# Kernel optimization log

Hardware: AMD Instinct MI355X
Metric: run time of the kernel (lower is better)

The kernel has to match this reference:

```python
import jax, jax.numpy as jnp
import numpy as np

N = 50000
E = 800000
EPS = 1e-5


def graph_conv(x, src, dst, ew, W_rel, b_rel, W_root):
    # PyG GraphConv (aggr='add'): lin_rel(sum_j e_ij * x_j) + lin_root(x_i)
    msg = x[src] * ew[:, None]                      # [E, F_in]
    agg = jax.ops.segment_sum(msg, dst, num_segments=N)  # [N, F_in]
    return agg @ W_rel.T + b_rel + x @ W_root.T


def batchnorm_relu(h, gamma, beta):
    mu = jnp.mean(h, axis=0)
    var = jnp.mean(jnp.square(h - mu), axis=0)
    hn = (h - mu) * jax.lax.rsqrt(var + EPS)
    return jax.nn.relu(hn * gamma + beta)


def setup_inputs() -> dict:
    key = jax.random.key(0)
    ks = jax.random.split(key, 16)
    d_in, h, d_out = 128, 256, 64

    def lin(k, fo, fi):
        return jax.random.normal(k, (fo, fi), jnp.float32) * (1.0 / np.sqrt(fi))

    return {
        "x": jax.random.normal(ks[0], (N, d_in), jnp.float32),
        "edge_index": jax.random.randint(ks[1], (2, E), 0, N, jnp.int32),
        "edge_weight": jax.random.uniform(ks[2], (E,), jnp.float32),
        "Wr0": lin(ks[3], h, d_in), "br0": jnp.zeros((h,), jnp.float32), "Wt0": lin(ks[4], h, d_in),
        "g0": jnp.ones((h,), jnp.float32), "be0": jnp.zeros((h,), jnp.float32),
        "Wr1": lin(ks[5], h, h), "br1": jnp.zeros((h,), jnp.float32), "Wt1": lin(ks[6], h, h),
        "g1": jnp.ones((h,), jnp.float32), "be1": jnp.zeros((h,), jnp.float32),
        "Wr2": lin(ks[7], d_out, h), "br2": jnp.zeros((d_out,), jnp.float32), "Wt2": lin(ks[8], d_out, h),
    }


def reference(x, edge_index, edge_weight, Wr0, br0, Wt0, g0, be0,
              Wr1, br1, Wt1, g1, be1, Wr2, br2, Wt2):
    src, dst = edge_index[0], edge_index[1]
    h = graph_conv(x, src, dst, edge_weight, Wr0, br0, Wt0)
    h = batchnorm_relu(h, g0, be0)
    h = graph_conv(h, src, dst, edge_weight, Wr1, br1, Wt1)
    h = batchnorm_relu(h, g1, be1)
    return graph_conv(h, src, dst, edge_weight, Wr2, br2, Wt2)
```

## Files before the change

### kernel.cpp

```cpp
#include <hip/hip_runtime.h>
#include <cstddef>
#include <cstdint>

#define SCAN_B 512

using bf16x8 = __attribute__((ext_vector_type(8))) short;
using f32x4  = __attribute__((ext_vector_type(4))) float;

__device__ __forceinline__ unsigned short f2bf(float f) {
    unsigned int u = __builtin_bit_cast(unsigned int, f);
    return (unsigned short)((u + 0x7FFFu + ((u >> 16) & 1u)) >> 16);
}
__device__ __forceinline__ float bf2f(unsigned short b) {
    unsigned int u = ((unsigned int)b) << 16;
    return __builtin_bit_cast(float, u);
}
__device__ __forceinline__ float i2f(int i) { return __builtin_bit_cast(float, i); }
__device__ __forceinline__ float u2f(unsigned int u) { return __builtin_bit_cast(float, u); }
__device__ __forceinline__ void gload_lds16(const void* g, void* l) {
    __builtin_amdgcn_global_load_lds((const __attribute__((address_space(1))) void*)g,
                                     (__attribute__((address_space(3))) void*)l, 16, 0, 0);
}

__global__ void hist_conv_k(const int* __restrict__ dst, int* __restrict__ counts,
                            int* __restrict__ rank, int E, int histBlocks,
                            const float* __restrict__ x, const float* __restrict__ Wr0,
                            const float* __restrict__ Wt0, const float* __restrict__ Wr1,
                            const float* __restrict__ Wt1, const float* __restrict__ Wr2,
                            const float* __restrict__ Wt2, unsigned short* __restrict__ x_bf,
                            unsigned short* __restrict__ Wr0b, unsigned short* __restrict__ Wt0b,
                            unsigned short* __restrict__ Wr1b, unsigned short* __restrict__ Wt1b,
                            unsigned short* __restrict__ Wr2b, unsigned short* __restrict__ Wt2b,
                            int n4x) {
    if ((int)blockIdx.x < histBlocks) {
        int e = blockIdx.x * 256 + threadIdx.x;
        if (e < E) rank[e] = atomicAdd(&counts[dst[e]], 1);
        return;
    }
    int j = (blockIdx.x - histBlocks) * 256 + threadIdx.x;
    const float* s;
    unsigned short* d;
    if (j < n4x) { s = x; d = x_bf; }
    else {
        j -= n4x;
        if (j < 8192) { s = Wr0; d = Wr0b; }
        else { j -= 8192;
        if (j < 8192) { s = Wt0; d = Wt0b; }
        else { j -= 8192;
        if (j < 16384) { s = Wr1; d = Wr1b; }
        else { j -= 16384;
        if (j < 16384) { s = Wt1; d = Wt1b; }
        else { j -= 16384;
        if (j < 4096) { s = Wr2; d = Wr2b; }
        else { j -= 4096;
        if (j >= 4096) return;
        s = Wt2; d = Wt2b; } } } } }
    }
    float4 v = reinterpret_cast<const float4*>(s)[j];
    ushort4 o;
    o.x = f2bf(v.x); o.y = f2bf(v.y); o.z = f2bf(v.z); o.w = f2bf(v.w);
    reinterpret_cast<ushort4*>(d)[j] = o;
}

__global__ void scan1_k(const int* __restrict__ counts, int* __restrict__ partial,
                        int* __restrict__ blocksum, int Nn) {
    __shared__ int sh[SCAN_B];
    int i = blockIdx.x * SCAN_B + threadIdx.x;
    int v = (i < Nn) ? counts[i] : 0;
    sh[threadIdx.x] = v;
    __syncthreads();
    for (int off = 1; off < SCAN_B; off <<= 1) {
        int t = (threadIdx.x >= (unsigned)off) ? sh[threadIdx.x - off] : 0;
        __syncthreads();
        sh[threadIdx.x] += t;
        __syncthreads();
    }
    if (i < Nn) partial[i] = sh[threadIdx.x];
    if (threadIdx.x == SCAN_B - 1) blocksum[blockIdx.x] = sh[threadIdx.x];
}

__global__ void scan3b_k(const int* __restrict__ partial, const int* __restrict__ blocksum,
                         int* __restrict__ offsets, int Nn) {
    __shared__ int add_s;
    int bx = blockIdx.x;
    if (threadIdx.x < 64) {
        int s = 0;
        for (int j = threadIdx.x; j < bx; j += 64) s += blocksum[j];
        #pragma unroll
        for (int off = 32; off > 0; off >>= 1) s += __shfl_down(s, off, 64);
        if (threadIdx.x == 0) add_s = s;
    }
    __syncthreads();
    int i = bx * SCAN_B + threadIdx.x;
    if (i >= Nn) return;
    offsets[i + 1] = partial[i] + add_s;
    if (i == 0) offsets[0] = 0;
}

__global__ void fill2_k(const int* __restrict__ src, const int* __restrict__ dst,
                        const float* __restrict__ ew, const int* __restrict__ offsets,
                        const int* __restrict__ rank, int2* __restrict__ e_sw, int E) {
    int e = blockIdx.x * blockDim.x + threadIdx.x;
    if (e >= E) return;
    int pos = offsets[dst[e]] + rank[e];
    e_sw[pos] = make_int2(src[e], __builtin_bit_cast(int, ew[e]));
}

__global__ void gather128_k(const unsigned short* __restrict__ x, const int* __restrict__ offsets,
                            const int2* __restrict__ e_sw, unsigned short* __restrict__ agg, int Nn) {
    int wid = __builtin_amdgcn_readfirstlane((blockIdx.x * blockDim.x + threadIdx.x) >> 6);
    int lane = threadIdx.x & 63;
    if (wid >= Nn) return;
    int p = offsets[wid], end = offsets[wid + 1];
    const char* xb = (const char*)x;
    const unsigned loff = lane * 4u;
    float a0 = 0.f, a1 = 0.f;
    for (; p + 8 <= end; p += 8) {
        int2 ee[8];
        #pragma unroll
        for (int i = 0; i < 8; ++i) ee[i] = e_sw[p + i];
        unsigned vv[8];
        #pragma unroll
        for (int i = 0; i < 8; ++i)
            vv[i] = *reinterpret_cast<const unsigned*>(xb + ((unsigned)ee[i].x * 256u + loff));
        #pragma unroll
        for (int i = 0; i < 8; ++i) {
            float w = i2f(ee[i].y);
            a0 += w * u2f(vv[i] << 16); a1 += w * u2f(vv[i] & 0xFFFF0000u);
        }
    }
    for (; p < end; ++p) {
        int2 e0 = e_sw[p];
        unsigned v0 = *reinterpret_cast<const unsigned*>(xb + ((unsigned)e0.x * 256u + loff));
        float w = i2f(e0.y);
        a0 += w * u2f(v0 << 16); a1 += w * u2f(v0 & 0xFFFF0000u);
    }
    unsigned o = (unsigned)f2bf(a0) | ((unsigned)f2bf(a1) << 16);
    *reinterpret_cast<unsigned*>(agg + (size_t)wid * 128 + lane * 2) = o;
}

__global__ void gather_bn_k(const unsigned short* __restrict__ h_raw,
                            const float* __restrict__ sums, const float* __restrict__ sumsq,
                            const float* __restrict__ g, const float* __restrict__ be,
                            const int* __restrict__ offsets, const int2* __restrict__ e_sw,
                            unsigned short* __restrict__ agg, unsigned short* __restrict__ hN,
                            float invN, int Nn) {
    const int lane = threadIdx.x & 63;
    const int bx = blockIdx.x;
    if (bx % 7 == 6) {
        int bidx = bx / 7;
        int nbn = (int)gridDim.x / 7;
        int total4 = Nn * 64;
        int stride = nbn * 256;
        for (int t = bidx * 256 + threadIdx.x; t < total4; t += stride) {
            int f0 = (t & 63) * 4;
            float4 sm = *reinterpret_cast<const float4*>(sums + f0);
            float4 sq = *reinterpret_cast<const float4*>(sumsq + f0);
            float4 gg = *reinterpret_cast<const float4*>(g + f0);
            float4 bb = *reinterpret_cast<const float4*>(be + f0);
            float smv[4] = {sm.x, sm.y, sm.z, sm.w};
            float sqv[4] = {sq.x, sq.y, sq.z, sq.w};
            float ggv[4] = {gg.x, gg.y, gg.z, gg.w};
            float bbv[4] = {bb.x, bb.y, bb.z, bb.w};
            ushort4 v = reinterpret_cast<const ushort4*>(h_raw)[t];
            unsigned short vv[4] = {v.x, v.y, v.z, v.w};
            ushort4 o;
            unsigned short* op = &o.x;
            #pragma unroll
            for (int c = 0; c < 4; ++c) {
                float mu = smv[c] * invN;
                float var = sqv[c] * invN - mu * mu;
                float sc = ggv[c] * rsqrtf(var + 1e-5f);
                float sh = bbv[c] - mu * sc;
                op[c] = f2bf(fmaxf(bf2f(vv[c]) * sc + sh, 0.f));
            }
            reinterpret_cast<ushort4*>(hN)[t] = o;
        }
        return;
    }
    int gidx = bx - (bx + 1) / 7;
    int wid = __builtin_amdgcn_readfirstlane((gidx * 256 + (int)threadIdx.x) >> 6);
    if (wid >= Nn) return;
    int f0 = lane * 4;
    float4 sm = *reinterpret_cast<const float4*>(sums + f0);
    float4 sq = *reinterpret_cast<const float4*>(sumsq + f0);
    float4 gg = *reinterpret_cast<const float4*>(g + f0);
    float4 bb = *reinterpret_cast<const float4*>(be + f0);
    float sc0, sc1, sc2, sc3, sh0, sh1, sh2, sh3;
    {
        float mu, var;
        mu = sm.x * invN; var = sq.x * invN - mu * mu; sc0 = gg.x * rsqrtf(var + 1e-5f); sh0 = bb.x - mu * sc0;
        mu = sm.y * invN; var = sq.y * invN - mu * mu; sc1 = gg.y * rsqrtf(var + 1e-5f); sh1 = bb.y - mu * sc1;
        mu = sm.z * invN; var = sq.z * invN - mu * mu; sc2 = gg.z * rsqrtf(var + 1e-5f); sh2 = bb.z - mu * sc2;
        mu = sm.w * invN; var = sq.w * invN - mu * mu; sc3 = gg.w * rsqrtf(var + 1e-5f); sh3 = bb.w - mu * sc3;
    }
    int p = offsets[wid], end = offsets[wid + 1];
    const char* xb = (const char*)h_raw;
    const unsigned loff = lane * 8u;
    float a0 = 0.f, a1 = 0.f, a2 = 0.f, a3 = 0.f;
    for (; p + 8 <= end; p += 8) {
        int2 ee[8];
        #pragma unroll
        for (int i = 0; i < 8; ++i) ee[i] = e_sw[p + i];
        uint2 vv[8];
        #pragma unroll
        for (int i = 0; i < 8; ++i)
            vv[i] = *reinterpret_cast<const uint2*>(xb + ((unsigned)ee[i].x * 512u + loff));
        #pragma unroll
        for (int i = 0; i < 8; ++i) {
            float w = i2f(ee[i].y);
            a0 += w * fmaxf(u2f(vv[i].x << 16) * sc0 + sh0, 0.f);
            a1 += w * fmaxf(u2f(vv[i].x & 0xFFFF0000u) * sc1 + sh1, 0.f);
            a2 += w * fmaxf(u2f(vv[i].y << 16) * sc2 + sh2, 0.f);
            a3 += w * fmaxf(u2f(vv[i].y & 0xFFFF0000u) * sc3 + sh3, 0.f);
        }
    }
    for (; p < end; ++p) {
        int2 e0 = e_sw[p];
        uint2 v0 = *reinterpret_cast<const uint2*>(xb + ((unsigned)e0.x * 512u + loff));
        float w = i2f(e0.y);
        a0 += w * fmaxf(u2f(v0.x << 16) * sc0 + sh0, 0.f);
        a1 += w * fmaxf(u2f(v0.x & 0xFFFF0000u) * sc1 + sh1, 0.f);
        a2 += w * fmaxf(u2f(v0.y << 16) * sc2 + sh2, 0.f);
        a3 += w * fmaxf(u2f(v0.y & 0xFFFF0000u) * sc3 + sh3, 0.f);
    }
    uint2 o;
    o.x = (unsigned)f2bf(a0) | ((unsigned)f2bf(a1) << 16);
    o.y = (unsigned)f2bf(a2) | ((unsigned)f2bf(a3) << 16);
    *reinterpret_cast<uint2*>(agg + (size_t)wid * 256 + lane * 4) = o;
}

__global__ void gather_out_k(const unsigned short* __restrict__ t, const float* __restrict__ root,
                             const int* __restrict__ offsets, const int2* __restrict__ e_sw,
                             float* __restrict__ out, int Nn) {
    int gt = blockIdx.x * blockDim.x + threadIdx.x;
    int node = gt >> 4;
    int li = gt & 15;
    if (node >= Nn) return;
    int p = offsets[node], end = offsets[node + 1];
    const char* tb = (const char*)t;
    const unsigned loff = li * 8u;
    float a0 = 0.f, a1 = 0.f, a2 = 0.f, a3 = 0.f;
    for (; p + 8 <= end; p += 8) {
        int2 ee[8];
        #pragma unroll
        for (int i = 0; i < 8; ++i) ee[i] = e_sw[p + i];
        uint2 vv[8];
        #pragma unroll
        for (int i = 0; i < 8; ++i)
            vv[i] = *reinterpret_cast<const uint2*>(tb + ((unsigned)ee[i].x * 128u + loff));
        #pragma unroll
        for (int i = 0; i < 8; ++i) {
            float w = i2f(ee[i].y);
            a0 += w * u2f(vv[i].x << 16); a1 += w * u2f(vv[i].x & 0xFFFF0000u);
            a2 += w * u2f(vv[i].y << 16); a3 += w * u2f(vv[i].y & 0xFFFF0000u);
        }
    }
    for (; p < end; ++p) {
        int2 e0 = e_sw[p];
        uint2 v0 = *reinterpret_cast<const uint2*>(tb + ((unsigned)e0.x * 128u + loff));
        float w = i2f(e0.y);
        a0 += w * u2f(v0.x << 16); a1 += w * u2f(v0.x & 0xFFFF0000u);
        a2 += w * u2f(v0.y << 16); a3 += w * u2f(v0.y & 0xFFFF0000u);
    }
    float4 r = *reinterpret_cast<const float4*>(root + (size_t)node * 64 + li * 4);
    float4 o = make_float4(r.x + a0, r.y + a1, r.z + a2, r.w + a3);
    *reinterpret_cast<float4*>(out + (size_t)node * 64 + li * 4) = o;
}

template<int K, int O, int MODE>
__global__ __launch_bounds__(512, 4) void gemm_mfma_k(
        const unsigned short* __restrict__ A, const unsigned short* __restrict__ Wa,
        const unsigned short* __restrict__ X, const unsigned short* __restrict__ Wb,
        const float* __restrict__ bias, unsigned short* __restrict__ out_bf,
        float* __restrict__ out_f, float* __restrict__ sums, float* __restrict__ sumsq,
        int Nn) {
    constexpr int BM = 128, BN = 128;
    constexpr int MI = 4;
    constexpr int OJ = 2;
    constexpr int KSTEPS = K / 32;
    constexpr int NT = (MODE == 0 ? 2 : 1) * KSTEPS;
    __shared__ unsigned short As[2][BM * 32];
    __shared__ unsigned short Bs[2][BN * 32];
    const int tid = threadIdx.x;
    const int w = tid >> 6, l = tid & 63;
    const int wr = w >> 2, wc = w & 3;
    const int lrow = l & 15, kgrp = l >> 4;
    int bx = blockIdx.x;
    bx = (bx & 7) * (gridDim.x >> 3) + (bx >> 3);
    const int m0 = bx * BM;
    const int n0 = blockIdx.y * BN;
    const int srow = tid >> 2, sslot = tid & 3;
    const int gslot = sslot ^ ((srow >> 1) & 3);

    auto stage = [&](int buf, int t) {
        int ph = t / KSTEPS;
        int k0 = (t % KSTEPS) * 32;
        const unsigned short* Ap = (MODE == 0 && ph) ? X : A;
        const unsigned short* Wp = (MODE == 0 && ph) ? Wb : Wa;
        gload_lds16(Ap + (size_t)(m0 + srow) * K + k0 + (gslot << 3), &As[buf][w * 512]);
        gload_lds16(Wp + (size_t)(n0 + srow) * K + k0 + (gslot << 3), &Bs[buf][w * 512]);
    };

    f32x4 acc[MI][OJ];
    #pragma unroll
    for (int i = 0; i < MI; ++i)
        #pragma unroll
        for (int j = 0; j < OJ; ++j) {
            f32x4 z = {0.f, 0.f, 0.f, 0.f};
            acc[i][j] = z;
        }

    stage(0, 0);
    __syncthreads();
    #pragma unroll
    for (int t = 0; t < NT; ++t) {
        const int cur = t & 1;
        if (t + 1 < NT) stage(cur ^ 1, t + 1);
        bf16x8 a[MI], b[OJ];
        #pragma unroll
        for (int mi = 0; mi < MI; ++mi) {
            int row = wr * 64 + mi * 16 + lrow;
            int slot = kgrp ^ ((row >> 1) & 3);
            a[mi] = *reinterpret_cast<const bf16x8*>(&As[cur][row * 32 + slot * 8]);
        }
        #pragma unroll
        for (int oj = 0; oj < OJ; ++oj) {
            int row = wc * 32 + oj * 16 + lrow;
            int slot = kgrp ^ ((row >> 1) & 3);
            b[oj] = *reinterpret_cast<const bf16x8*>(&Bs[cur][row * 32 + slot * 8]);
        }
        #pragma unroll
        for (int mi = 0; mi < MI; ++mi)
            #pragma unroll
            for (int oj = 0; oj < OJ; ++oj)
                acc[mi][oj] = __builtin_amdgcn_mfma_f32_16x16x32_bf16(
                    a[mi], b[oj], acc[mi][oj], 0, 0, 0);
        __syncthreads();
    }

    #pragma unroll
    for (int oj = 0; oj < OJ; ++oj) {
        int col = n0 + wc * 32 + oj * 16 + lrow;
        float bcol = bias[col];
        float s = 0.f, q = 0.f;
        #pragma unroll
        for (int mi = 0; mi < MI; ++mi) {
            #pragma unroll
            for (int r = 0; r < 4; ++r) {
                int row = m0 + wr * 64 + mi * 16 + kgrp * 4 + r;
                float v = acc[mi][oj][r] + bcol;
                if (row < Nn) {
                    out_bf[(size_t)row * O + col] = f2bf(v);
                    s += v; q += v * v;
                }
            }
        }
        s += __shfl_xor(s, 16, 64); q += __shfl_xor(q, 16, 64);
        s += __shfl_xor(s, 32, 64); q += __shfl_xor(q, 32, 64);
        if (kgrp == 0) {
            atomicAdd(&sums[col], s);
            atomicAdd(&sumsq[col], q);
        }
    }
}

template<int K>
__global__ __launch_bounds__(512, 4) void gemm2_bn_k(
        const unsigned short* __restrict__ A, const unsigned short* __restrict__ Wa,
        const float* __restrict__ sums, const float* __restrict__ sumsq,
        const float* __restrict__ g, const float* __restrict__ be,
        const float* __restrict__ bias, unsigned short* __restrict__ t_bf,
        float* __restrict__ root, float invN, int Nn) {
    constexpr int BM = 128, BN = 128;
    constexpr int MI = 4, OJ = 2;
    constexpr int NT = K / 32;
    __shared__ unsigned short As[2][BM * 32];
    __shared__ unsigned short Bs[2][BN * 32];
    const int tid = threadIdx.x;
    const int w = tid >> 6, l = tid & 63;
    const int wr = w >> 2, wc = w & 3;
    const int lrow = l & 15, kgrp = l >> 4;
    int bx = blockIdx.x;
    bx = (bx & 7) * (gridDim.x >> 3) + (bx >> 3);
    const int m0 = bx * BM;
    const int srow = tid >> 2, sslot = tid & 3;
    const int gslot = sslot ^ ((srow >> 1) & 3);

    auto stageW = [&](int buf, int t) {
        gload_lds16(Wa + (size_t)srow * K + t * 32 + (gslot << 3), &Bs[buf][w * 512]);
    };
    auto loadA = [&](int t) -> bf16x8 {
        return *reinterpret_cast<const bf16x8*>(A + (size_t)(m0 + srow) * K + t * 32 + (gslot << 3));
    };
    auto writeA = [&](int buf, int t, bf16x8 raw) {
        int f0 = t * 32 + (gslot << 3);
        bf16x8 o;
        #pragma unroll
        for (int j = 0; j < 8; ++j) {
            int f = f0 + j;
            float mu = sums[f] * invN;
            float var = sumsq[f] * invN - mu * mu;
            float sc = g[f] * rsqrtf(var + 1e-5f);
            float sh = be[f] - mu * sc;
            float v = bf2f((unsigned short)raw[j]) * sc + sh;
            o[j] = (short)f2bf(fmaxf(v, 0.f));
        }
        *reinterpret_cast<bf16x8*>(&As[buf][tid * 8]) = o;
    };

    f32x4 acc[MI][OJ];
    #pragma unroll
    for (int i = 0; i < MI; ++i)
        #pragma unroll
        for (int j = 0; j < OJ; ++j) {
            f32x4 z = {0.f, 0.f, 0.f, 0.f};
            acc[i][j] = z;
        }

    {
        bf16x8 r0 = loadA(0);
        stageW(0, 0);
        writeA(0, 0, r0);
    }
    __syncthreads();
    #pragma unroll
    for (int t = 0; t < NT; ++t) {
        const int cur = t & 1;
        bf16x8 nxt;
        if (t + 1 < NT) { nxt = loadA(t + 1); stageW(cur ^ 1, t + 1); }
        bf16x8 a[MI], b[OJ];
        #pragma unroll
        for (int mi = 0; mi < MI; ++mi) {
            int row = wr * 64 + mi * 16 + lrow;
            int slot = kgrp ^ ((row >> 1) & 3);
            a[mi] = *reinterpret_cast<const bf16x8*>(&As[cur][row * 32 + slot * 8]);
        }
        #pragma unroll
        for (int oj = 0; oj < OJ; ++oj) {
            int row = wc * 32 + oj * 16 + lrow;
            int slot = kgrp ^ ((row >> 1) & 3);
            b[oj] = *reinterpret_cast<const bf16x8*>(&Bs[cur][row * 32 + slot * 8]);
        }
        #pragma unroll
        for (int mi = 0; mi < MI; ++mi)
            #pragma unroll
            for (int oj = 0; oj < OJ; ++oj)
                acc[mi][oj] = __builtin_amdgcn_mfma_f32_16x16x32_bf16(
                    a[mi], b[oj], acc[mi][oj], 0, 0, 0);
        if (t + 1 < NT) writeA(cur ^ 1, t + 1, nxt);
        __syncthreads();
    }

    #pragma unroll
    for (int oj = 0; oj < OJ; ++oj) {
        int col = wc * 32 + oj * 16 + lrow;
        #pragma unroll
        for (int mi = 0; mi < MI; ++mi) {
            #pragma unroll
            for (int r = 0; r < 4; ++r) {
                int row = m0 + wr * 64 + mi * 16 + kgrp * 4 + r;
                if (row < Nn) {
                    if (col < 64)
                        t_bf[(size_t)row * 64 + col] = f2bf(acc[mi][oj][r]);
                    else
                        root[(size_t)row * 64 + (col - 64)] = acc[mi][oj][r] + bias[col - 64];
                }
            }
        }
    }
}

extern "C" void kernel_launch(void* const* d_in, const int* in_sizes, int n_in,
                              void* d_out, int out_size, void* d_ws, size_t ws_size,
                              hipStream_t stream) {
    const float* x   = (const float*)d_in[0];
    const int*   ei  = (const int*)d_in[1];
    const float* ew  = (const float*)d_in[2];
    const float* Wr0 = (const float*)d_in[3];
    const float* br0 = (const float*)d_in[4];
    const float* Wt0 = (const float*)d_in[5];
    const float* g0  = (const float*)d_in[6];
    const float* be0 = (const float*)d_in[7];
    const float* Wr1 = (const float*)d_in[8];
    const float* br1 = (const float*)d_in[9];
    const float* Wt1 = (const float*)d_in[10];
    const float* g1  = (const float*)d_in[11];
    const float* be1 = (const float*)d_in[12];
    const float* Wr2 = (const float*)d_in[13];
    const float* br2 = (const float*)d_in[14];
    const float* Wt2 = (const float*)d_in[15];

    const int E  = in_sizes[2];
    const int Nn = in_sizes[0] / 128;
    const size_t NP = 50176;
    const int* src = ei;
    const int* dst = ei + E;

    unsigned short* x_bf   = (unsigned short*)d_ws;
    unsigned short* agg_bf = x_bf + NP * 128;
    unsigned short* h0N    = agg_bf + NP * 256;
    unsigned short* h1N    = h0N + NP * 256;
    unsigned short* h_bf   = h1N + NP * 256;
    unsigned short* t_bf   = h_bf + NP * 256;
    unsigned short* wbf    = t_bf + NP * 64;
    unsigned short* Wr0b = wbf;
    unsigned short* Wt0b = wbf + 32768;
    unsigned short* Wr1b = wbf + 65536;
    unsigned short* Wt1b = wbf + 131072;
    unsigned short* W2cat = wbf + 196608;
    float* root  = (float*)(wbf + 229376);
    int2*  e_sw  = (int2*)(root + NP * 64);
    float* stats = (float*)(e_sw + E);
    int*   counts  = (int*)(stats + 4096);
    int*   partial = counts + Nn;
    int*   blocksum = partial + Nn;
    int*   rank    = blocksum + 512;
    int*   offsets = rank + E;

    dim3 blk(256);
    const int nbScan = (Nn + SCAN_B - 1) / SCAN_B;
    const float invN = 1.0f / (float)Nn;
    const int n4x = Nn * 32;
    const int histBlocks = (E + 255) / 256;
    const int convBlocks = (n4x + 57344 + 255) / 256;

    hipMemsetAsync(stats, 0, (4096 + (size_t)Nn) * sizeof(float), stream);

    hist_conv_k<<<dim3(histBlocks + convBlocks), blk, 0, stream>>>(
        dst, counts, rank, E, histBlocks,
        x, Wr0, Wt0, Wr1, Wt1, Wr2, Wt2,
        x_bf, Wr0b, Wt0b, Wr1b, Wt1b, W2cat, W2cat + 16384, n4x);
    scan1_k<<<dim3(nbScan), dim3(SCAN_B), 0, stream>>>(counts, partial, blocksum, Nn);
    scan3b_k<<<dim3(nbScan), dim3(SCAN_B), 0, stream>>>(partial, blocksum, offsets, Nn);
    fill2_k<<<dim3(histBlocks), blk, 0, stream>>>(src, dst, ew, offsets, rank, e_sw, E);

    const int gatherBlocks = (Nn * 64 + 255) / 256;

    gather128_k<<<dim3(gatherBlocks), blk, 0, stream>>>(x_bf, offsets, e_sw, agg_bf, Nn);
    gemm_mfma_k<128, 256, 0><<<dim3(NP / 128, 2), dim3(512), 0, stream>>>(
        agg_bf, Wr0b, x_bf, Wt0b, br0, h_bf, nullptr, stats + 0, stats + 256, Nn);

    gather_bn_k<<<dim3(14584), blk, 0, stream>>>(
        h_bf, stats + 0, stats + 256, g0, be0, offsets, e_sw,
        agg_bf, h0N, invN, Nn);

    gemm_mfma_k<256, 256, 0><<<dim3(NP / 128, 2), dim3(512), 0, stream>>>(
        agg_bf, Wr1b, h0N, Wt1b, br1, h_bf, nullptr, stats + 1024, stats + 1280, Nn);

    gemm2_bn_k<256><<<dim3(NP / 128, 1), dim3(512), 0, stream>>>(
        h_bf, W2cat, stats + 1024, stats + 1280, g1, be1, br2, t_bf, root, invN, Nn);
    gather_out_k<<<dim3((Nn * 16 + 255) / 256), blk, 0, stream>>>(
        t_bf, root, offsets, e_sw, (float*)d_out, Nn);
}
```

Measured before the change: 293.5 us.

## Fuse layer-0 BN+ReLU into layer-1 GEMM root operand and precompute BN scales in LDS

Result: faster. 281.3 us (-4.1%).

```diff
diff --git a/kernel.cpp b/kernel.cpp
--- a/kernel.cpp
+++ b/kernel.cpp
@@ -143,43 +143,9 @@
                             const float* __restrict__ sums, const float* __restrict__ sumsq,
                             const float* __restrict__ g, const float* __restrict__ be,
                             const int* __restrict__ offsets, const int2* __restrict__ e_sw,
-                            unsigned short* __restrict__ agg, unsigned short* __restrict__ hN,
-                            float invN, int Nn) {
+                            unsigned short* __restrict__ agg, float invN, int Nn) {
     const int lane = threadIdx.x & 63;
-    const int bx = blockIdx.x;
-    if (bx % 7 == 6) {
-        int bidx = bx / 7;
-        int nbn = (int)gridDim.x / 7;
-        int total4 = Nn * 64;
-        int stride = nbn * 256;
-        for (int t = bidx * 256 + threadIdx.x; t < total4; t += stride) {
-            int f0 = (t & 63) * 4;
-            float4 sm = *reinterpret_cast<const float4*>(sums + f0);
-            float4 sq = *reinterpret_cast<const float4*>(sumsq + f0);
-            float4 gg = *reinterpret_cast<const float4*>(g + f0);
-            float4 bb = *reinterpret_cast<const float4*>(be + f0);
-            float smv[4] = {sm.x, sm.y, sm.z, sm.w};
-            float sqv[4] = {sq.x, sq.y, sq.z, sq.w};
-            float ggv[4] = {gg.x, gg.y, gg.z, gg.w};
-            float bbv[4] = {bb.x, bb.y, bb.z, bb.w};
-            ushort4 v = reinterpret_cast<const ushort4*>(h_raw)[t];
-            unsigned short vv[4] = {v.x, v.y, v.z, v.w};
-            ushort4 o;
-            unsigned short* op = &o.x;
-            #pragma unroll
-            for (int c = 0; c < 4; ++c) {
-                float mu = smv[c] * invN;
-                float var = sqv[c] * invN - mu * mu;
-                float sc = ggv[c] * rsqrtf(var + 1e-5f);
-                float sh = bbv[c] - mu * sc;
-                op[c] = f2bf(fmaxf(bf2f(vv[c]) * sc + sh, 0.f));
-            }
-            reinterpret_cast<ushort4*>(hN)[t] = o;
-        }
-        return;
-    }
-    int gidx = bx - (bx + 1) / 7;
-    int wid = __builtin_amdgcn_readfirstlane((gidx * 256 + (int)threadIdx.x) >> 6);
+    int wid = __builtin_amdgcn_readfirstlane((blockIdx.x * blockDim.x + threadIdx.x) >> 6);
     if (wid >= Nn) return;
     int f0 = lane * 4;
     float4 sm = *reinterpret_cast<const float4*>(sums + f0);
@@ -268,18 +234,16 @@
     *reinterpret_cast<float4*>(out + (size_t)node * 64 + li * 4) = o;
 }
 
-template<int K, int O, int MODE>
-__global__ __launch_bounds__(512, 4) void gemm_mfma_k(
+template<int K, int O>
+__global__ __launch_bounds__(512, 4) void gemm0_k(
         const unsigned short* __restrict__ A, const unsigned short* __restrict__ Wa,
         const unsigned short* __restrict__ X, const unsigned short* __restrict__ Wb,
         const float* __restrict__ bias, unsigned short* __restrict__ out_bf,
-        float* __restrict__ out_f, float* __restrict__ sums, float* __restrict__ sumsq,
-        int Nn) {
+        float* __restrict__ sums, float* __restrict__ sumsq, int Nn) {
     constexpr int BM = 128, BN = 128;
-    constexpr int MI = 4;
-    constexpr int OJ = 2;
+    constexpr int MI = 4, OJ = 2;
     constexpr int KSTEPS = K / 32;
-    constexpr int NT = (MODE == 0 ? 2 : 1) * KSTEPS;
+    constexpr int NT = 2 * KSTEPS;
     __shared__ unsigned short As[2][BM * 32];
     __shared__ unsigned short Bs[2][BN * 32];
     const int tid = threadIdx.x;
@@ -296,8 +260,8 @@
     auto stage = [&](int buf, int t) {
         int ph = t / KSTEPS;
         int k0 = (t % KSTEPS) * 32;
-        const unsigned short* Ap = (MODE == 0 && ph) ? X : A;
-        const unsigned short* Wp = (MODE == 0 && ph) ? Wb : Wa;
+        const unsigned short* Ap = ph ? X : A;
+        const unsigned short* Wp = ph ? Wb : Wa;
         gload_lds16(Ap + (size_t)(m0 + srow) * K + k0 + (gslot << 3), &As[buf][w * 512]);
         gload_lds16(Wp + (size_t)(n0 + srow) * K + k0 + (gslot << 3), &Bs[buf][w * 512]);
     };
@@ -361,6 +325,135 @@
         if (kgrp == 0) {
             atomicAdd(&sums[col], s);
             atomicAdd(&sumsq[col], q);
+        }
+    }
+}
+
+template<int K, int O>
+__global__ __launch_bounds__(512, 4) void gemm1_bn_k(
+        const unsigned short* __restrict__ A, const unsigned short* __restrict__ Wa,
+        const unsigned short* __restrict__ X, const unsigned short* __restrict__ Wb,
+        const float* __restrict__ sums0, const float* __restrict__ sumsq0,
+        const float* __restrict__ g0, const float* __restrict__ be0,
+        const float* __restrict__ bias, unsigned short* __restrict__ out_bf,
+        float* __restrict__ sums1, float* __restrict__ sumsq1, float invN, int Nn) {
+    constexpr int BM = 128, BN = 128;
+    constexpr int MI = 4, OJ = 2;
+    constexpr int KSTEPS = K / 32;
+    constexpr int NT = 2 * KSTEPS;
+    __shared__ unsigned short As[2][BM * 32];
+    __shared__ unsigned short Bs[2][BN * 32];
+    __shared__ float scs[256], shs[256];
+    const int tid = threadIdx.x;
+    const int w = tid >> 6, l = tid & 63;
+    const int wr = w >> 2, wc = w & 3;
+    const int lrow = l & 15, kgrp = l >> 4;
+    int bx = blockIdx.x;
+    bx = (bx & 7) * (gridDim.x >> 3) + (bx >> 3);
+    const int m0 = bx * BM;
+    const int n0 = blockIdx.y * BN;
+    const int srow = tid >> 2, sslot = tid & 3;
+    const int gslot = sslot ^ ((srow >> 1) & 3);
+
+    auto stageB = [&](int buf, int t) {
+        int k0 = (t % KSTEPS) * 32;
+        const unsigned short* Wp = (t < KSTEPS) ? Wa : Wb;
+        gload_lds16(Wp + (size_t)(n0 + srow) * K + k0 + (gslot << 3), &Bs[buf][w * 512]);
+    };
+    auto stageA = [&](int buf, int t) {
+        int k0 = t * 32;
+        gload_lds16(A + (size_t)(m0 + srow) * K + k0 + (gslot << 3), &As[buf][w * 512]);
+    };
+    auto loadX = [&](int t) -> bf16x8 {
+        int k0 = (t - KSTEPS) * 32;
+        return *reinterpret_cast<const bf16x8*>(X + (size_t)(m0 + srow) * K + k0 + (gslot << 3));
+    };
+    auto writeX = [&](int buf, int t, bf16x8 raw) {
+        int f0 = (t - KSTEPS) * 32 + (gslot << 3);
+        bf16x8 o;
+        #pragma unroll
+        for (int j = 0; j < 8; ++j) {
+            float v = bf2f((unsigned short)raw[j]) * scs[f0 + j] + shs[f0 + j];
+            o[j] = (short)f2bf(fmaxf(v, 0.f));
+        }
+        *reinterpret_cast<bf16x8*>(&As[buf][tid * 8]) = o;
+    };
+
+    if (tid < 256) {
+        float mu = sums0[tid] * invN;
+        float var = sumsq0[tid] * invN - mu * mu;
+        float sc = g0[tid] * rsqrtf(var + 1e-5f);
+        scs[tid] = sc;
+        shs[tid] = be0[tid] - mu * sc;
+    }
+
+    f32x4 acc[MI][OJ];
+    #pragma unroll
+    for (int i = 0; i < MI; ++i)
+        #pragma unroll
+        for (int j = 0; j < OJ; ++j) {
+            f32x4 z = {0.f, 0.f, 0.f, 0.f};
+            acc[i][j] = z;
+        }
+
+    stageB(0, 0);
+    stageA(0, 0);
+    __syncthreads();
+    #pragma unroll
+    for (int t = 0; t < NT; ++t) {
+        const int cur = t & 1;
+        bf16x8 nxt;
+        const bool nxtReg = (t + 1 < NT) && (t + 1 >= KSTEPS);
+        if (t + 1 < NT) {
+            stageB(cur ^ 1, t + 1);
+            if (t + 1 < KSTEPS) stageA(cur ^ 1, t + 1);
+            else nxt = loadX(t + 1);
+        }
+        bf16x8 a[MI], b[OJ];
+        #pragma unroll
+        for (int mi = 0; mi < MI; ++mi) {
+            int row = wr * 64 + mi * 16 + lrow;
+            int slot = kgrp ^ ((row >> 1) & 3);
+            a[mi] = *reinterpret_cast<const bf16x8*>(&As[cur][row * 32 + slot * 8]);
+        }
+        #pragma unroll
+        for (int oj = 0; oj < OJ; ++oj) {
+            int row = wc * 32 + oj * 16 + lrow;
+            int slot = kgrp ^ ((row >> 1) & 3);
+            b[oj] = *reinterpret_cast<const bf16x8*>(&Bs[cur][row * 32 + slot * 8]);
+        }
+        #pragma unroll
+        for (int mi = 0; mi < MI; ++mi)
+            #pragma unroll
+            for (int oj = 0; oj < OJ; ++oj)
+                acc[mi][oj] = __builtin_amdgcn_mfma_f32_16x16x32_bf16(
+                    a[mi], b[oj], acc[mi][oj], 0, 0, 0);
+        if (nxtReg) writeX(cur ^ 1, t + 1, nxt);
+        __syncthreads();
+    }
+
+    #pragma unroll
+    for (int oj = 0; oj < OJ; ++oj) {
+        int col = n0 + wc * 32 + oj * 16 + lrow;
+        float bcol = bias[col];
+        float s = 0.f, q = 0.f;
+        #pragma unroll
+        for (int mi = 0; mi < MI; ++mi) {
+            #pragma unroll
+            for (int r = 0; r < 4; ++r) {
+                int row = m0 + wr * 64 + mi * 16 + kgrp * 4 + r;
+                float v = acc[mi][oj][r] + bcol;
+                if (row < Nn) {
+                    out_bf[(size_t)row * O + col] = f2bf(v);
+                    s += v; q += v * v;
+                }
+            }
+        }
+        s += __shfl_xor(s, 16, 64); q += __shfl_xor(q, 16, 64);
+        s += __shfl_xor(s, 32, 64); q += __shfl_xor(q, 32, 64);
+        if (kgrp == 0) {
+            atomicAdd(&sums1[col], s);
+            atomicAdd(&sumsq1[col], q);
         }
     }
 }
@@ -377,6 +470,7 @@
     constexpr int NT = K / 32;
     __shared__ unsigned short As[2][BM * 32];
     __shared__ unsigned short Bs[2][BN * 32];
+    __shared__ float scs[256], shs[256];
     const int tid = threadIdx.x;
     const int w = tid >> 6, l = tid & 63;
     const int wr = w >> 2, wc = w & 3;
@@ -398,16 +492,19 @@
         bf16x8 o;
         #pragma unroll
         for (int j = 0; j < 8; ++j) {
-            int f = f0 + j;
-            float mu = sums[f] * invN;
-            float var = sumsq[f] * invN - mu * mu;
-            float sc = g[f] * rsqrtf(var + 1e-5f);
-            float sh = be[f] - mu * sc;
-            float v = bf2f((unsigned short)raw[j]) * sc + sh;
+            float v = bf2f((unsigned short)raw[j]) * scs[f0 + j] + shs[f0 + j];
             o[j] = (short)f2bf(fmaxf(v, 0.f));
         }
         *reinterpret_cast<bf16x8*>(&As[buf][tid * 8]) = o;
     };
+
+    if (tid < 256) {
+        float mu = sums[tid] * invN;
+        float var = sumsq[tid] * invN - mu * mu;
+        float sc = g[tid] * rsqrtf(var + 1e-5f);
+        scs[tid] = sc;
+        shs[tid] = be[tid] - mu * sc;
+    }
 
     f32x4 acc[MI][OJ];
     #pragma unroll
@@ -418,11 +515,10 @@
             acc[i][j] = z;
         }
 
-    {
-        bf16x8 r0 = loadA(0);
-        stageW(0, 0);
-        writeA(0, 0, r0);
-    }
+    bf16x8 r0 = loadA(0);
+    stageW(0, 0);
+    __syncthreads();
+    writeA(0, 0, r0);
     __syncthreads();
     #pragma unroll
     for (int t = 0; t < NT; ++t) {
@@ -499,8 +595,7 @@
 
     unsigned short* x_bf   = (unsigned short*)d_ws;
     unsigned short* agg_bf = x_bf + NP * 128;
-    unsigned short* h0N    = agg_bf + NP * 256;
-    unsigned short* h1N    = h0N + NP * 256;
+    unsigned short* h1N    = agg_bf + NP * 256;
     unsigned short* h_bf   = h1N + NP * 256;
     unsigned short* t_bf   = h_bf + NP * 256;
     unsigned short* wbf    = t_bf + NP * 64;
@@ -538,18 +633,17 @@
     const int gatherBlocks = (Nn * 64 + 255) / 256;
 
     gather128_k<<<dim3(gatherBlocks), blk, 0, stream>>>(x_bf, offsets, e_sw, agg_bf, Nn);
-    gemm_mfma_k<128, 256, 0><<<dim3(NP / 128, 2), dim3(512), 0, stream>>>(
-        agg_bf, Wr0b, x_bf, Wt0b, br0, h_bf, nullptr, stats + 0, stats + 256, Nn);
-
-    gather_bn_k<<<dim3(14584), blk, 0, stream>>>(
-        h_bf, stats + 0, stats + 256, g0, be0, offsets, e_sw,
-        agg_bf, h0N, invN, Nn);
-
-    gemm_mfma_k<256, 256, 0><<<dim3(NP / 128, 2), dim3(512), 0, stream>>>(
-        agg_bf, Wr1b, h0N, Wt1b, br1, h_bf, nullptr, stats + 1024, stats + 1280, Nn);
+    gemm0_k<128, 256><<<dim3(NP / 128, 2), dim3(512), 0, stream>>>(
+        agg_bf, Wr0b, x_bf, Wt0b, br0, h_bf, stats + 0, stats + 256, Nn);
+
+    gather_bn_k<<<dim3(gatherBlocks), blk, 0, stream>>>(
+        h_bf, stats + 0, stats + 256, g0, be0, offsets, e_sw, agg_bf, invN, Nn);
+    gemm1_bn_k<256, 256><<<dim3(NP / 128, 2), dim3(512), 0, stream>>>(
+        agg_bf, Wr1b, h_bf, Wt1b, stats + 0, stats + 256, g0, be0,
+        br1, h1N, stats + 1024, stats + 1280, invN, Nn);
 
     gemm2_bn_k<256><<<dim3(NP / 128, 1), dim3(512), 0, stream>>>(
-        h_bf, W2cat, stats + 1024, stats + 1280, g1, be1, br2, t_bf, root, invN, Nn);
+        h1N, W2cat, stats + 1024, stats + 1280, g1, be1, br2, t_bf, root, invN, Nn);
     gather_out_k<<<dim3((Nn * 16 + 255) / 256), blk, 0, stream>>>(
         t_bf, root, offsets, e_sw, (float*)d_out, Nn);
 }
```
